# Performance work log

Measured on AMD Instinct MI355X. Metric: run time of the kernel, lower is better.

Reference implementation:

```python
import jax, jax.numpy as jnp
import numpy as np

B, H, W = 32, 768, 768
POS_THR = 0.1
NEG_RATIO = 3
TOPK_NO_POS = 500


def setup_inputs() -> dict:
    key = jax.random.key(0)
    k1, k2, k3 = jax.random.split(key, 3)
    pred = jax.random.uniform(k1, (B, H, W, 2), dtype=jnp.float32)
    region_scores = jax.random.uniform(k2, (B, H, W), dtype=jnp.float32) ** 16
    affinity_scores = jax.random.uniform(k3, (B, H, W), dtype=jnp.float32) ** 16
    return {"pred": pred, "region_scores": region_scores, "affinity_scores": affinity_scores}


def _single_image_loss(pre_loss, label):
    # Vectorized OHEM: replaces the per-sample Python loop + torch.topk.
    b = pre_loss.shape[0]
    loss = pre_loss.reshape(b, -1)   # [B, N]
    lab = label.reshape(b, -1)       # [B, N]
    n = loss.shape[1]
    pos = lab >= POS_THR             # [B, N] bool
    p = jnp.sum(pos, axis=1)         # positive pixel count per sample
    pos_sum = jnp.sum(jnp.where(pos, loss, 0.0), axis=1)
    posi_loss = jnp.where(p > 0, pos_sum / jnp.maximum(p, 1).astype(loss.dtype), 0.0)
    # Negatives sorted descending; -inf pushes positives to the tail.
    # When p == 0 the mask is all-False so this sorts the full loss vector,
    # matching torch.topk(pre_loss[i], 500).
    neg_vals = jnp.where(pos, -jnp.inf, loss)
    sorted_desc = jnp.flip(jnp.sort(neg_vals, axis=1), axis=1)
    nn = n - p                       # negative count
    # mean of all negatives when nn < 3p == mean of top-min(nn,3p); else top-3p
    k = jnp.where(p > 0, jnp.minimum(nn, NEG_RATIO * p), TOPK_NO_POS)
    csum = jnp.cumsum(jnp.where(jnp.isfinite(sorted_desc), sorted_desc, 0.0), axis=1)
    topk_sum = jnp.take_along_axis(csum, jnp.maximum(k - 1, 0)[:, None], axis=1)[:, 0]
    nega_loss = jnp.where(k > 0, topk_sum / jnp.maximum(k, 1).astype(loss.dtype), 0.0)
    return jnp.sum(posi_loss + nega_loss)


def reference(pred, region_scores, affinity_scores):
    p_gh = pred[..., 0]
    p_gah = pred[..., 1]
    loss1 = (p_gh - region_scores) ** 2   # MSELoss(reduction='none')
    loss2 = (p_gah - affinity_scores) ** 2
    char_loss = _single_image_loss(loss1, region_scores)
    affi_loss = _single_image_loss(loss2, affinity_scores)
    b = pred.shape[0]
    return char_loss / b + affi_loss / b
```

## Files before the change

kernel.cpp:

```cpp
#include <hip/hip_runtime.h>


constexpr int   BATCH   = 32;
constexpr int   NPS     = 768 * 768;
constexpr int   CH2     = BATCH * 2;
constexpr int   EPB     = 16384;
constexpr int   BX      = NPS / EPB;
constexpr float POS_THR_F = 0.1f;
constexpr unsigned TOPK_NO_POS = 500u;
constexpr int   NB1     = 2048;
constexpr int   CAP     = 131072;
constexpr int   CAPB    = 1024;

__global__ __launch_bounds__(256, 4) void k_hist(
    const float4* __restrict__ pred4,
    const float4* __restrict__ reg4,
    const float4* __restrict__ aff4,
    unsigned* __restrict__ h1c, float* __restrict__ h1s,
    unsigned* __restrict__ pcnt, float* __restrict__ psum)
{
    __shared__ unsigned sc0[NB1], sc1[NB1];
    __shared__ float    ss0[NB1], ss1[NB1];
    __shared__ unsigned wpc[8];
    __shared__ float    wps[8];
    for (int j = threadIdx.x; j < NB1; j += 256) { sc0[j]=0u; sc1[j]=0u; ss0[j]=0.f; ss1[j]=0.f; }
    __syncthreads();

    const int  b   = blockIdx.y;
    const int  tid = threadIdx.x;
    constexpr int ITERS = EPB / 1024;
    long idx4 = (((long)b * NPS + (long)blockIdx.x * EPB) >> 2) + tid;

    unsigned pc0 = 0, pc1 = 0;
    float    ps0 = 0.f, ps1 = 0.f;

    float4 r = reg4[idx4], a = aff4[idx4];
    float4 pA = pred4[idx4 * 2], pB = pred4[idx4 * 2 + 1];

    for (int i = 0; i < ITERS; ++i) {
        float4 rn, an, pAn, pBn;
        if (i + 1 < ITERS) {
            const long nx = idx4 + 256;
            rn = reg4[nx]; an = aff4[nx]; pAn = pred4[nx * 2]; pBn = pred4[nx * 2 + 1];
        }
#define DO_PIX(RR, AA, PG, PA) do {                                           \
        float d0 = (PG) - (RR); float v0 = d0 * d0;                           \
        if ((RR) >= POS_THR_F) { pc0++; ps0 += v0; }                          \
        else { unsigned ky = __float_as_uint(v0) >> 19;                       \
               atomicAdd(&sc0[ky], 1u); unsafeAtomicAdd(&ss0[ky], v0); }      \
        float d1 = (PA) - (AA); float v1 = d1 * d1;                           \
        if ((AA) >= POS_THR_F) { pc1++; ps1 += v1; }                          \
        else { unsigned ky = __float_as_uint(v1) >> 19;                       \
               atomicAdd(&sc1[ky], 1u); unsafeAtomicAdd(&ss1[ky], v1); }      \
    } while (0)
        DO_PIX(r.x, a.x, pA.x, pA.y);
        DO_PIX(r.y, a.y, pA.z, pA.w);
        DO_PIX(r.z, a.z, pB.x, pB.y);
        DO_PIX(r.w, a.w, pB.z, pB.w);
#undef DO_PIX
        idx4 += 256; r = rn; a = an; pA = pAn; pB = pBn;
    }
    __syncthreads();

    for (int j = tid; j < NB1; j += 256) {
        unsigned c0 = sc0[j];
        if (c0) { atomicAdd(&h1c[(b*2+0)*NB1 + j], c0); unsafeAtomicAdd(&h1s[(b*2+0)*NB1 + j], ss0[j]); }
        unsigned c1 = sc1[j];
        if (c1) { atomicAdd(&h1c[(b*2+1)*NB1 + j], c1); unsafeAtomicAdd(&h1s[(b*2+1)*NB1 + j], ss1[j]); }
    }
    for (int o = 32; o > 0; o >>= 1) {
        pc0 += __shfl_down(pc0, o); ps0 += __shfl_down(ps0, o);
        pc1 += __shfl_down(pc1, o); ps1 += __shfl_down(ps1, o);
    }
    const int wid = tid >> 6, lane = tid & 63;
    if (lane == 0) { wpc[wid] = pc0; wps[wid] = ps0; wpc[4+wid] = pc1; wps[4+wid] = ps1; }
    __syncthreads();
    if (tid == 0) {
        unsigned t0 = 0, t1 = 0; float s0 = 0.f, s1 = 0.f;
        for (int q = 0; q < 4; ++q) { t0 += wpc[q]; s0 += wps[q]; t1 += wpc[4+q]; s1 += wps[4+q]; }
        atomicAdd(&pcnt[b*2+0], t0); unsafeAtomicAdd(&psum[b*2+0], s0);
        atomicAdd(&pcnt[b*2+1], t1); unsafeAtomicAdd(&psum[b*2+1], s1);
    }
}

template<int NBINS>
__device__ __forceinline__ void select_counts(
    const unsigned* cnt, unsigned k, unsigned& outBin, unsigned& outRem)
{
    constexpr int PER = NBINS / 256;
    const int t = threadIdx.x;
    unsigned lc[PER];
#pragma unroll
    for (int j = 0; j < PER; ++j) lc[j] = cnt[t*PER + j];
    unsigned lsum = 0;
#pragma unroll
    for (int j = 0; j < PER; ++j) lsum += lc[j];

    __shared__ unsigned part[256];
    __shared__ unsigned s_bin, s_rem;
    part[t] = lsum;
    __syncthreads();
    for (int off = 1; off < 256; off <<= 1) {
        unsigned v = (t + off < 256) ? part[t + off] : 0u;
        __syncthreads();
        part[t] += v;
        __syncthreads();
    }
    unsigned cum = (t + 1 < 256) ? part[t + 1] : 0u;
#pragma unroll
    for (int j = PER - 1; j >= 0; --j) {
        unsigned c = lc[j];
        if (cum < k && k <= cum + c) { s_bin = (unsigned)(t * PER + j); s_rem = k - cum; }
        cum += c;
    }
    __syncthreads();
    outBin = s_bin; outRem = s_rem;
}

template<int NBINS>
__device__ __forceinline__ void select_counts_sums(
    const unsigned* cnt, const float* sums,
    unsigned k, unsigned& outBin, unsigned& outRem, double& outSum)
{
    constexpr int PER = NBINS / 256;
    const int t = threadIdx.x;
    unsigned lc[PER]; float lf[PER];
#pragma unroll
    for (int j = 0; j < PER; ++j) { lc[j] = cnt[t*PER + j]; lf[j] = sums[t*PER + j]; }
    unsigned lsum = 0;
#pragma unroll
    for (int j = 0; j < PER; ++j) lsum += lc[j];

    __shared__ unsigned part[256];
    __shared__ unsigned s_bin, s_rem;
    __shared__ double   wsum[4];
    part[t] = lsum;
    __syncthreads();
    for (int off = 1; off < 256; off <<= 1) {
        unsigned v = (t + off < 256) ? part[t + off] : 0u;
        __syncthreads();
        part[t] += v;
        __syncthreads();
    }
    unsigned cum = (t + 1 < 256) ? part[t + 1] : 0u;
#pragma unroll
    for (int j = PER - 1; j >= 0; --j) {
        unsigned c = lc[j];
        if (cum < k && k <= cum + c) { s_bin = (unsigned)(t * PER + j); s_rem = k - cum; }
        cum += c;
    }
    __syncthreads();
    const unsigned bin = s_bin;
    double ds = 0.0;
#pragma unroll
    for (int j = 0; j < PER; ++j)
        if ((unsigned)(t * PER + j) > bin) ds += (double)lf[j];
    for (int o = 32; o > 0; o >>= 1) ds += __shfl_down(ds, o);
    const int wid = t >> 6, lane = t & 63;
    if (lane == 0) wsum[wid] = ds;
    __syncthreads();
    if (t == 0) ds = wsum[0] + wsum[1] + wsum[2] + wsum[3];
    outBin = bin; outRem = s_rem; outSum = ds;
}

__global__ __launch_bounds__(256) void k_scan1(
    const unsigned* __restrict__ h1c, const float* __restrict__ h1s,
    const unsigned* __restrict__ pcnt, const float* __restrict__ psum,
    unsigned* __restrict__ T1, unsigned* __restrict__ rem1,
    unsigned* __restrict__ kk, float* __restrict__ posi,
    double* __restrict__ sumAbove)
{
    const int idx = blockIdx.x;
    const unsigned p  = pcnt[idx];
    const unsigned nn = (unsigned)NPS - p;
    const unsigned k  = p ? ((nn < 3u*p) ? nn : 3u*p) : TOPK_NO_POS;
    if (threadIdx.x == 0) {
        kk[idx]   = k;
        posi[idx] = p ? (psum[idx] / (float)p) : 0.0f;
    }
    if (k == 0u) {
        if (threadIdx.x == 0) { T1[idx] = 0xFFFFFFFFu; rem1[idx] = 0u; sumAbove[idx] = 0.0; }
        return;
    }
    unsigned bin, rem; double s;
    select_counts_sums<NB1>(h1c + idx*NB1, h1s + idx*NB1, k, bin, rem, s);
    if (threadIdx.x == 0) { T1[idx] = bin; rem1[idx] = rem; sumAbove[idx] = s; }
}

__global__ __launch_bounds__(256, 4) void k_compact(
    const float4* __restrict__ pred4,
    const float4* __restrict__ reg4,
    const float4* __restrict__ aff4,
    const unsigned* __restrict__ T1,
    float* __restrict__ cbuf, unsigned* __restrict__ ccnt)
{
    __shared__ float    lb0[CAPB], lb1[CAPB];
    __shared__ unsigned lcnt[2];
    __shared__ unsigned sbase[2];
    if (threadIdx.x < 2) lcnt[threadIdx.x] = 0u;
    __syncthreads();

    const int b = blockIdx.y;
    const unsigned t1r = T1[b*2+0], t1a = T1[b*2+1];
    const int tid = threadIdx.x, lane = tid & 63;
    float*    gb0 = cbuf + (size_t)(b*2+0) * CAP;
    float*    gb1 = cbuf + (size_t)(b*2+1) * CAP;
    unsigned* gc0 = ccnt + b*2+0;
    unsigned* gc1 = ccnt + b*2+1;

    auto proc = [&](float tgt, float pg, unsigned t1,
                    unsigned* lcnt_p, float* lbuf, unsigned* gcnt, float* gbuf) {
        if (tgt >= POS_THR_F) return;
        const float d = pg - tgt;
        const float v = d * d;
        if ((__float_as_uint(v) >> 19) != t1) return;
        const unsigned long long m = __ballot(true);
        const int ldr = __ffsll(m) - 1;
        const unsigned pre = (unsigned)__popcll(m & ((1ull << lane) - 1ull));
        unsigned base = 0;
        if (lane == ldr) base = atomicAdd(lcnt_p, (unsigned)__popcll(m));
        base = __shfl(base, ldr);
        const unsigned ix = base + pre;
        if (ix < (unsigned)CAPB) lbuf[ix] = v;
        else { unsigned g = atomicAdd(gcnt, 1u); if (g < (unsigned)CAP) gbuf[g] = v; }
    };

    constexpr int ITERS = EPB / 1024;
    long idx4 = (((long)b * NPS + (long)blockIdx.x * EPB) >> 2) + tid;
    for (int i = 0; i < ITERS; ++i) {
        float4 rn, an, pAn, pBn;
        if (i + 1 < ITERS) {
            const long nx = idx4 + 256;
            rn = reg4[nx]; an = aff4[nx]; pAn = pred4[nx * 2]; pBn = pred4[nx * 2 + 1];
        } else {
            rn = reg4[idx4]; an = aff4[idx4]; pAn = pred4[idx4*2]; pBn = pred4[idx4*2+1];
        }
        const float4 r  = (i == 0) ? reg4[idx4] : rn;
        (void)r;
        const float4 rr = reg4[idx4];
        const float4 aa = aff4[idx4];
        const float4 pA = pred4[idx4*2];
        const float4 pB = pred4[idx4*2+1];
        proc(rr.x, pA.x, t1r, &lcnt[0], lb0, gc0, gb0);
        proc(rr.y, pA.z, t1r, &lcnt[0], lb0, gc0, gb0);
        proc(rr.z, pB.x, t1r, &lcnt[0], lb0, gc0, gb0);
        proc(rr.w, pB.z, t1r, &lcnt[0], lb0, gc0, gb0);
        proc(aa.x, pA.y, t1a, &lcnt[1], lb1, gc1, gb1);
        proc(aa.y, pA.w, t1a, &lcnt[1], lb1, gc1, gb1);
        proc(aa.z, pB.y, t1a, &lcnt[1], lb1, gc1, gb1);
        proc(aa.w, pB.w, t1a, &lcnt[1], lb1, gc1, gb1);
        idx4 += 256;
    }
    __syncthreads();

    const unsigned lc0 = lcnt[0] < (unsigned)CAPB ? lcnt[0] : (unsigned)CAPB;
    const unsigned lc1 = lcnt[1] < (unsigned)CAPB ? lcnt[1] : (unsigned)CAPB;
    if (tid == 0)      sbase[0] = lc0 ? atomicAdd(gc0, lc0) : 0u;
    else if (tid == 1) sbase[1] = lc1 ? atomicAdd(gc1, lc1) : 0u;
    __syncthreads();
    for (unsigned i = tid; i < lc0; i += 256) {
        unsigned g = sbase[0] + i;
        if (g < (unsigned)CAP) gb0[g] = lb0[i];
    }
    for (unsigned i = tid; i < lc1; i += 256) {
        unsigned g = sbase[1] + i;
        if (g < (unsigned)CAP) gb1[g] = lb1[i];
    }
}

__global__ __launch_bounds__(256) void k_refine(
    const float* __restrict__ cbuf, const unsigned* __restrict__ ccnt,
    const unsigned* __restrict__ T1, const unsigned* __restrict__ rem1,
    const unsigned* __restrict__ kk, const float* __restrict__ posi,
    const double* __restrict__ sumAbove,
    float* __restrict__ contrib)
{
    const int ch = blockIdx.x;
    const unsigned k = kk[ch];
    if (k == 0u) {
        if (threadIdx.x == 0) contrib[ch] = posi[ch];
        return;
    }
    unsigned cnt = ccnt[ch];
    if (cnt > (unsigned)CAP) cnt = (unsigned)CAP;
    const float* buf = cbuf + (size_t)ch * CAP;
    const int tid = threadIdx.x;

    __shared__ unsigned hA[NB1];
    __shared__ unsigned hB[256];
    __shared__ double   wsum[4];
    for (int j = tid; j < NB1; j += 256) hA[j] = 0u;
    __syncthreads();
    for (unsigned i = tid; i < cnt; i += 256) {
        const unsigned bt = __float_as_uint(buf[i]);
        atomicAdd(&hA[(bt >> 8) & 2047u], 1u);
    }
    __syncthreads();
    unsigned T2, rem2;
    select_counts<NB1>(hA, rem1[ch], T2, rem2);

    hB[tid] = 0u;
    __syncthreads();
    for (unsigned i = tid; i < cnt; i += 256) {
        const unsigned bt = __float_as_uint(buf[i]);
        if (((bt >> 8) & 2047u) == T2) atomicAdd(&hB[bt & 255u], 1u);
    }
    __syncthreads();
    unsigned T3, rem3;
    select_counts<256>(hB, rem2, T3, rem3);

    const float t = __uint_as_float((T1[ch] << 19) | (T2 << 8) | T3);
    double s = 0.0;
    for (unsigned i = tid; i < cnt; i += 256) {
        const float v = buf[i];
        if (v > t) s += (double)v;
    }
    for (int o = 32; o > 0; o >>= 1) s += __shfl_down(s, o);
    const int wid = tid >> 6, lane = tid & 63;
    if (lane == 0) wsum[wid] = s;
    __syncthreads();
    if (tid == 0) {
        const double stop = wsum[0] + wsum[1] + wsum[2] + wsum[3];
        const double nega = (sumAbove[ch] + stop + (double)rem3 * (double)t) / (double)k;
        contrib[ch] = (float)((double)posi[ch] + nega);
    }
}

__global__ void k_reduce(const float* __restrict__ contrib, float* __restrict__ out)
{
    double v = (double)contrib[threadIdx.x];
    for (int o = 32; o > 0; o >>= 1) v += __shfl_down(v, o);
    if (threadIdx.x == 0) out[0] = (float)(v / (double)BATCH);
}

extern "C" void kernel_launch(void* const* d_in, const int* in_sizes, int n_in,
                              void* d_out, int out_size, void* d_ws, size_t ws_size,
                              hipStream_t stream)
{
    (void)in_sizes; (void)n_in; (void)out_size; (void)ws_size;
    const float4* pred4 = (const float4*)d_in[0];
    const float4* reg4  = (const float4*)d_in[1];
    const float4* aff4  = (const float4*)d_in[2];

    char* w = (char*)d_ws;
    unsigned* h1c  = (unsigned*)w;
    float*    h1s  = (float*)(h1c + (size_t)CH2 * NB1);
    unsigned* pcnt = (unsigned*)(h1s + (size_t)CH2 * NB1);
    float*    psum = (float*)(pcnt + CH2);
    unsigned* T1   = (unsigned*)(psum + CH2);
    unsigned* rem1 = T1 + CH2;
    unsigned* kk   = rem1 + CH2;
    float*    posi = (float*)(kk + CH2);
    float*    contrib = posi + CH2;
    unsigned* ccnt = (unsigned*)(contrib + CH2);
    double*   sumAbove = (double*)(ccnt + CH2);
    const size_t hdr_bytes = (size_t)((char*)(sumAbove + CH2) - w);

    float* cbuf = (float*)(w + ((size_t)2 << 20));

    hipMemsetAsync(d_ws, 0, hdr_bytes, stream);

    dim3 grid(BX, BATCH);
    k_hist<<<grid, 256, 0, stream>>>(pred4, reg4, aff4, h1c, h1s, pcnt, psum);
    k_scan1<<<CH2, 256, 0, stream>>>(h1c, h1s, pcnt, psum, T1, rem1, kk, posi, sumAbove);
    k_compact<<<grid, 256, 0, stream>>>(pred4, reg4, aff4, T1, cbuf, ccnt);
    k_refine<<<CH2, 256, 0, stream>>>(cbuf, ccnt, T1, rem1, kk, posi, sumAbove, contrib);
    k_reduce<<<1, 64, 0, stream>>>(contrib, (float*)d_out);
}
```

Measured before the change: 482.0 us.

## Drop per-bin sum histogram; accumulate above-threshold sums during compaction

```diff
diff --git a/kernel.cpp b/kernel.cpp
--- a/kernel.cpp
+++ b/kernel.cpp
@@ -12,18 +12,17 @@
 constexpr int   CAP     = 131072;
 constexpr int   CAPB    = 1024;
 
-__global__ __launch_bounds__(256, 4) void k_hist(
+__global__ __launch_bounds__(256, 6) void k_hist(
     const float4* __restrict__ pred4,
     const float4* __restrict__ reg4,
     const float4* __restrict__ aff4,
-    unsigned* __restrict__ h1c, float* __restrict__ h1s,
+    unsigned* __restrict__ h1c,
     unsigned* __restrict__ pcnt, float* __restrict__ psum)
 {
     __shared__ unsigned sc0[NB1], sc1[NB1];
-    __shared__ float    ss0[NB1], ss1[NB1];
     __shared__ unsigned wpc[8];
     __shared__ float    wps[8];
-    for (int j = threadIdx.x; j < NB1; j += 256) { sc0[j]=0u; sc1[j]=0u; ss0[j]=0.f; ss1[j]=0.f; }
+    for (int j = threadIdx.x; j < NB1; j += 256) { sc0[j] = 0u; sc1[j] = 0u; }
     __syncthreads();
 
     const int  b   = blockIdx.y;
@@ -46,12 +45,10 @@
 #define DO_PIX(RR, AA, PG, PA) do {                                           \
         float d0 = (PG) - (RR); float v0 = d0 * d0;                           \
         if ((RR) >= POS_THR_F) { pc0++; ps0 += v0; }                          \
-        else { unsigned ky = __float_as_uint(v0) >> 19;                       \
-               atomicAdd(&sc0[ky], 1u); unsafeAtomicAdd(&ss0[ky], v0); }      \
+        else atomicAdd(&sc0[__float_as_uint(v0) >> 19], 1u);                  \
         float d1 = (PA) - (AA); float v1 = d1 * d1;                           \
         if ((AA) >= POS_THR_F) { pc1++; ps1 += v1; }                          \
-        else { unsigned ky = __float_as_uint(v1) >> 19;                       \
-               atomicAdd(&sc1[ky], 1u); unsafeAtomicAdd(&ss1[ky], v1); }      \
+        else atomicAdd(&sc1[__float_as_uint(v1) >> 19], 1u);                  \
     } while (0)
         DO_PIX(r.x, a.x, pA.x, pA.y);
         DO_PIX(r.y, a.y, pA.z, pA.w);
@@ -64,9 +61,9 @@
 
     for (int j = tid; j < NB1; j += 256) {
         unsigned c0 = sc0[j];
-        if (c0) { atomicAdd(&h1c[(b*2+0)*NB1 + j], c0); unsafeAtomicAdd(&h1s[(b*2+0)*NB1 + j], ss0[j]); }
+        if (c0) atomicAdd(&h1c[(b*2+0)*NB1 + j], c0);
         unsigned c1 = sc1[j];
-        if (c1) { atomicAdd(&h1c[(b*2+1)*NB1 + j], c1); unsafeAtomicAdd(&h1s[(b*2+1)*NB1 + j], ss1[j]); }
+        if (c1) atomicAdd(&h1c[(b*2+1)*NB1 + j], c1);
     }
     for (int o = 32; o > 0; o >>= 1) {
         pc0 += __shfl_down(pc0, o); ps0 += __shfl_down(ps0, o);
@@ -117,58 +114,11 @@
     outBin = s_bin; outRem = s_rem;
 }
 
-template<int NBINS>
-__device__ __forceinline__ void select_counts_sums(
-    const unsigned* cnt, const float* sums,
-    unsigned k, unsigned& outBin, unsigned& outRem, double& outSum)
-{
-    constexpr int PER = NBINS / 256;
-    const int t = threadIdx.x;
-    unsigned lc[PER]; float lf[PER];
-#pragma unroll
-    for (int j = 0; j < PER; ++j) { lc[j] = cnt[t*PER + j]; lf[j] = sums[t*PER + j]; }
-    unsigned lsum = 0;
-#pragma unroll
-    for (int j = 0; j < PER; ++j) lsum += lc[j];
-
-    __shared__ unsigned part[256];
-    __shared__ unsigned s_bin, s_rem;
-    __shared__ double   wsum[4];
-    part[t] = lsum;
-    __syncthreads();
-    for (int off = 1; off < 256; off <<= 1) {
-        unsigned v = (t + off < 256) ? part[t + off] : 0u;
-        __syncthreads();
-        part[t] += v;
-        __syncthreads();
-    }
-    unsigned cum = (t + 1 < 256) ? part[t + 1] : 0u;
-#pragma unroll
-    for (int j = PER - 1; j >= 0; --j) {
-        unsigned c = lc[j];
-        if (cum < k && k <= cum + c) { s_bin = (unsigned)(t * PER + j); s_rem = k - cum; }
-        cum += c;
-    }
-    __syncthreads();
-    const unsigned bin = s_bin;
-    double ds = 0.0;
-#pragma unroll
-    for (int j = 0; j < PER; ++j)
-        if ((unsigned)(t * PER + j) > bin) ds += (double)lf[j];
-    for (int o = 32; o > 0; o >>= 1) ds += __shfl_down(ds, o);
-    const int wid = t >> 6, lane = t & 63;
-    if (lane == 0) wsum[wid] = ds;
-    __syncthreads();
-    if (t == 0) ds = wsum[0] + wsum[1] + wsum[2] + wsum[3];
-    outBin = bin; outRem = s_rem; outSum = ds;
-}
-
 __global__ __launch_bounds__(256) void k_scan1(
-    const unsigned* __restrict__ h1c, const float* __restrict__ h1s,
+    const unsigned* __restrict__ h1c,
     const unsigned* __restrict__ pcnt, const float* __restrict__ psum,
     unsigned* __restrict__ T1, unsigned* __restrict__ rem1,
-    unsigned* __restrict__ kk, float* __restrict__ posi,
-    double* __restrict__ sumAbove)
+    unsigned* __restrict__ kk, float* __restrict__ posi)
 {
     const int idx = blockIdx.x;
     const unsigned p  = pcnt[idx];
@@ -179,24 +129,26 @@
         posi[idx] = p ? (psum[idx] / (float)p) : 0.0f;
     }
     if (k == 0u) {
-        if (threadIdx.x == 0) { T1[idx] = 0xFFFFFFFFu; rem1[idx] = 0u; sumAbove[idx] = 0.0; }
+        if (threadIdx.x == 0) { T1[idx] = 0xFFFFFFFFu; rem1[idx] = 0u; }
         return;
     }
-    unsigned bin, rem; double s;
-    select_counts_sums<NB1>(h1c + idx*NB1, h1s + idx*NB1, k, bin, rem, s);
-    if (threadIdx.x == 0) { T1[idx] = bin; rem1[idx] = rem; sumAbove[idx] = s; }
-}
-
-__global__ __launch_bounds__(256, 4) void k_compact(
+    unsigned bin, rem;
+    select_counts<NB1>(h1c + idx*NB1, k, bin, rem);
+    if (threadIdx.x == 0) { T1[idx] = bin; rem1[idx] = rem; }
+}
+
+__global__ __launch_bounds__(256, 6) void k_compact(
     const float4* __restrict__ pred4,
     const float4* __restrict__ reg4,
     const float4* __restrict__ aff4,
     const unsigned* __restrict__ T1,
-    float* __restrict__ cbuf, unsigned* __restrict__ ccnt)
+    float* __restrict__ cbuf, unsigned* __restrict__ ccnt,
+    double* __restrict__ sumAbove)
 {
     __shared__ float    lb0[CAPB], lb1[CAPB];
     __shared__ unsigned lcnt[2];
     __shared__ unsigned sbase[2];
+    __shared__ float    wred[8];
     if (threadIdx.x < 2) lcnt[threadIdx.x] = 0u;
     __syncthreads();
 
@@ -207,13 +159,16 @@
     float*    gb1 = cbuf + (size_t)(b*2+1) * CAP;
     unsigned* gc0 = ccnt + b*2+0;
     unsigned* gc1 = ccnt + b*2+1;
-
-    auto proc = [&](float tgt, float pg, unsigned t1,
+    float rs0 = 0.f, rs1 = 0.f;
+
+    auto proc = [&](float tgt, float pg, unsigned t1, float& rs,
                     unsigned* lcnt_p, float* lbuf, unsigned* gcnt, float* gbuf) {
         if (tgt >= POS_THR_F) return;
         const float d = pg - tgt;
         const float v = d * d;
-        if ((__float_as_uint(v) >> 19) != t1) return;
+        const unsigned key = __float_as_uint(v) >> 19;
+        if (key > t1) { rs += v; return; }
+        if (key != t1) return;
         const unsigned long long m = __ballot(true);
         const int ldr = __ffsll(m) - 1;
         const unsigned pre = (unsigned)__popcll(m & ((1ull << lane) - 1ull));
@@ -227,29 +182,25 @@
 
     constexpr int ITERS = EPB / 1024;
     long idx4 = (((long)b * NPS + (long)blockIdx.x * EPB) >> 2) + tid;
+
+    float4 r = reg4[idx4], a = aff4[idx4];
+    float4 pA = pred4[idx4 * 2], pB = pred4[idx4 * 2 + 1];
+
     for (int i = 0; i < ITERS; ++i) {
         float4 rn, an, pAn, pBn;
         if (i + 1 < ITERS) {
             const long nx = idx4 + 256;
             rn = reg4[nx]; an = aff4[nx]; pAn = pred4[nx * 2]; pBn = pred4[nx * 2 + 1];
-        } else {
-            rn = reg4[idx4]; an = aff4[idx4]; pAn = pred4[idx4*2]; pBn = pred4[idx4*2+1];
         }
-        const float4 r  = (i == 0) ? reg4[idx4] : rn;
-        (void)r;
-        const float4 rr = reg4[idx4];
-        const float4 aa = aff4[idx4];
-        const float4 pA = pred4[idx4*2];
-        const float4 pB = pred4[idx4*2+1];
-        proc(rr.x, pA.x, t1r, &lcnt[0], lb0, gc0, gb0);
-        proc(rr.y, pA.z, t1r, &lcnt[0], lb0, gc0, gb0);
-        proc(rr.z, pB.x, t1r, &lcnt[0], lb0, gc0, gb0);
-        proc(rr.w, pB.z, t1r, &lcnt[0], lb0, gc0, gb0);
-        proc(aa.x, pA.y, t1a, &lcnt[1], lb1, gc1, gb1);
-        proc(aa.y, pA.w, t1a, &lcnt[1], lb1, gc1, gb1);
-        proc(aa.z, pB.y, t1a, &lcnt[1], lb1, gc1, gb1);
-        proc(aa.w, pB.w, t1a, &lcnt[1], lb1, gc1, gb1);
-        idx4 += 256;
+        proc(r.x, pA.x, t1r, rs0, &lcnt[0], lb0, gc0, gb0);
+        proc(r.y, pA.z, t1r, rs0, &lcnt[0], lb0, gc0, gb0);
+        proc(r.z, pB.x, t1r, rs0, &lcnt[0], lb0, gc0, gb0);
+        proc(r.w, pB.z, t1r, rs0, &lcnt[0], lb0, gc0, gb0);
+        proc(a.x, pA.y, t1a, rs1, &lcnt[1], lb1, gc1, gb1);
+        proc(a.y, pA.w, t1a, rs1, &lcnt[1], lb1, gc1, gb1);
+        proc(a.z, pB.y, t1a, rs1, &lcnt[1], lb1, gc1, gb1);
+        proc(a.w, pB.w, t1a, rs1, &lcnt[1], lb1, gc1, gb1);
+        idx4 += 256; r = rn; a = an; pA = pAn; pB = pBn;
     }
     __syncthreads();
 
@@ -265,6 +216,16 @@
     for (unsigned i = tid; i < lc1; i += 256) {
         unsigned g = sbase[1] + i;
         if (g < (unsigned)CAP) gb1[g] = lb1[i];
+    }
+    for (int o = 32; o > 0; o >>= 1) { rs0 += __shfl_down(rs0, o); rs1 += __shfl_down(rs1, o); }
+    const int wid = tid >> 6;
+    if (lane == 0) { wred[wid] = rs0; wred[4+wid] = rs1; }
+    __syncthreads();
+    if (tid == 0) {
+        float s0 = wred[0]+wred[1]+wred[2]+wred[3];
+        float s1 = wred[4]+wred[5]+wred[6]+wred[7];
+        unsafeAtomicAdd(&sumAbove[b*2+0], (double)s0);
+        unsafeAtomicAdd(&sumAbove[b*2+1], (double)s1);
     }
 }
 
@@ -344,8 +305,7 @@
 
     char* w = (char*)d_ws;
     unsigned* h1c  = (unsigned*)w;
-    float*    h1s  = (float*)(h1c + (size_t)CH2 * NB1);
-    unsigned* pcnt = (unsigned*)(h1s + (size_t)CH2 * NB1);
+    unsigned* pcnt = h1c + (size_t)CH2 * NB1;
     float*    psum = (float*)(pcnt + CH2);
     unsigned* T1   = (unsigned*)(psum + CH2);
     unsigned* rem1 = T1 + CH2;
@@ -356,14 +316,14 @@
     double*   sumAbove = (double*)(ccnt + CH2);
     const size_t hdr_bytes = (size_t)((char*)(sumAbove + CH2) - w);
 
-    float* cbuf = (float*)(w + ((size_t)2 << 20));
+    float* cbuf = (float*)(w + ((size_t)1 << 20));
 
     hipMemsetAsync(d_ws, 0, hdr_bytes, stream);
 
     dim3 grid(BX, BATCH);
-    k_hist<<<grid, 256, 0, stream>>>(pred4, reg4, aff4, h1c, h1s, pcnt, psum);
-    k_scan1<<<CH2, 256, 0, stream>>>(h1c, h1s, pcnt, psum, T1, rem1, kk, posi, sumAbove);
-    k_compact<<<grid, 256, 0, stream>>>(pred4, reg4, aff4, T1, cbuf, ccnt);
+    k_hist<<<grid, 256, 0, stream>>>(pred4, reg4, aff4, h1c, pcnt, psum);
+    k_scan1<<<CH2, 256, 0, stream>>>(h1c, pcnt, psum, T1, rem1, kk, posi);
+    k_compact<<<grid, 256, 0, stream>>>(pred4, reg4, aff4, T1, cbuf, ccnt, sumAbove);
     k_refine<<<CH2, 256, 0, stream>>>(cbuf, ccnt, T1, rem1, kk, posi, sumAbove, contrib);
     k_reduce<<<1, 64, 0, stream>>>(contrib, (float*)d_out);
 }
```

Result: faster. 397.2 us (-17.6%).
